# Kernel tuning notes

Hardware: AMD Instinct MI355X
Metric: run time of the kernel (lower is better)

## Reference

```python
import jax, jax.numpy as jnp
import numpy as np

DIM, HEADS = 1024, 16
B, N = 2, 2048


def setup_inputs() -> dict:
    key = jax.random.key(0)
    ks = jax.random.split(key, 8)
    d = DIM // HEADS
    return {
        "x": jax.random.normal(ks[0], (B, N, DIM), dtype=jnp.float32),
        "w_qkv": jax.random.normal(ks[1], (DIM, 3 * DIM), dtype=jnp.float32) * (DIM ** -0.5),
        "w_out": jax.random.normal(ks[2], (DIM, DIM), dtype=jnp.float32) * (DIM ** -0.5),
        "b_out": jnp.zeros((DIM,), dtype=jnp.float32),
        "void_q": jax.random.normal(ks[3], (1, HEADS, 1, d), dtype=jnp.float32),
        "void_k": jax.random.normal(ks[4], (1, HEADS, 1, d), dtype=jnp.float32),
        "void_v": jax.random.normal(ks[5], (1, HEADS, 1, d), dtype=jnp.float32),
        "attention_trace": jax.random.uniform(ks[6], (HEADS, 1, 1), dtype=jnp.float32),
        "temperature_factor": jax.random.normal(ks[7], (HEADS, 1, 1), dtype=jnp.float32),
    }


def reference(x, w_qkv, w_out, b_out, void_q, void_k, void_v,
              attention_trace, temperature_factor):
    b, n, dim = x.shape
    h = void_q.shape[1]
    d = dim // h

    qkv = x @ w_qkv  # [b, n, 3*dim]
    q, k, v = jnp.split(qkv, 3, axis=-1)

    def to_heads(t):
        return t.reshape(b, n, h, d).transpose(0, 2, 1, 3)  # b h n d

    q, k, v = to_heads(q), to_heads(k), to_heads(v)

    # append the void token to q, k, v -> seq length n+1
    q = jnp.concatenate([q, jnp.broadcast_to(void_q, (b, h, 1, d))], axis=2)
    k = jnp.concatenate([k, jnp.broadcast_to(void_k, (b, h, 1, d))], axis=2)
    v = jnp.concatenate([v, jnp.broadcast_to(void_v, (b, h, 1, d))], axis=2)

    # NOTE: original scales by full dim**-0.5, not head-dim
    dots = jnp.einsum('bhid,bhjd->bhij', q, k) * (dim ** -0.5)
    # void-to-void bias of +10 at index [n, n]
    dots = dots.at[:, :, n, n].add(10.0)

    # stateful per-head temperature (trace is a buffer, treated as input)
    temperature = jnp.maximum(1.0 + jnp.abs(attention_trace) * temperature_factor, 1.0)  # [h,1,1]
    attn = jax.nn.softmax(dots / temperature, axis=-1)  # [b, h, n+1, n+1]

    out = jnp.einsum('bhij,bhjd->bhid', attn, v)[:, :, :n, :]  # drop void row
    out = out.transpose(0, 2, 1, 3).reshape(b, n, dim)  # b n (h d)
    return out @ w_out + b_out
```

## Files before the change

### kernel.cpp

```cpp
#include <hip/hip_runtime.h>
#include <stdint.h>

#define DIMF   1024
#define HEADS  16
#define HD     64
#define BB     2
#define NN     2048
#define NKP    2112
#define NTILE  33

typedef __attribute__((ext_vector_type(8))) __bf16 bf16x8;
typedef __attribute__((ext_vector_type(4))) float  f32x4;

__device__ __forceinline__ float b2f(uint16_t h) {
  union { uint32_t u; float f; } v; v.u = ((uint32_t)h) << 16; return v.f;
}
__device__ __forceinline__ uint16_t f2b(float f) {
  union { float f; uint32_t u; } v; v.f = f;
  uint32_t r = v.u + 0x7FFFu + ((v.u >> 16) & 1u);
  return (uint16_t)(r >> 16);
}

__device__ __forceinline__ void gl_lds16(const void* g, void* l) {
  __builtin_amdgcn_global_load_lds(
      (const __attribute__((address_space(1))) void*)g,
      (__attribute__((address_space(3))) void*)l, 16, 0, 0);
}

__global__ __launch_bounds__(256) void cvt_f32_bf16(const float* __restrict__ src,
                                                    uint16_t* __restrict__ dst, int n4) {
  int i = blockIdx.x * 256 + threadIdx.x;
  if (i < n4) {
    float4 v = *(const float4*)&src[i * 4];
    uint16_t* d = dst + i * 4;
    d[0] = f2b(v.x); d[1] = f2b(v.y); d[2] = f2b(v.z); d[3] = f2b(v.w);
  }
}

__global__ __launch_bounds__(256) void transpose_k(const float* __restrict__ src,
                                                   uint16_t* __restrict__ dst, int M, int N) {
  __shared__ uint16_t tile[32][33];
  int bx = blockIdx.x * 32, by = blockIdx.y * 32;
  int x = threadIdx.x, y0 = threadIdx.y;
#pragma unroll
  for (int i = 0; i < 32; i += 8)
    tile[y0 + i][x] = f2b(src[(size_t)(by + y0 + i) * N + bx + x]);
  __syncthreads();
#pragma unroll
  for (int i = 0; i < 32; i += 8)
    dst[(size_t)(bx + y0 + i) * M + by + x] = tile[x][y0 + i];
}

__global__ __launch_bounds__(256) void fill_void(const float* __restrict__ vk,
                                                 const float* __restrict__ vv,
                                                 uint16_t* __restrict__ k_ws,
                                                 uint16_t* __restrict__ vt_ws) {
  int idx = blockIdx.x * 256 + threadIdx.x;
  int dd = idx & 63;
  int r  = (idx >> 6) & 63;
  int bh = idx >> 12;
  int h  = bh & (HEADS - 1);
  uint16_t kv  = (r == 0) ? f2b(vk[h * HD + dd]) : (uint16_t)0;
  uint16_t vvv = (r == 0) ? f2b(vv[h * HD + dd]) : (uint16_t)0;
  k_ws[((size_t)bh * NKP + NN + r) * HD + dd]  = kv;
  vt_ws[((size_t)bh * HD + dd) * NKP + NN + r] = vvv;
}

template<int EPI>
__global__ __launch_bounds__(256) void gemm_bt(const uint16_t* __restrict__ A,
                                               const uint16_t* __restrict__ Bt,
                                               int K, int Nout,
                                               uint16_t* __restrict__ o0,
                                               uint16_t* __restrict__ o1,
                                               uint16_t* __restrict__ o2,
                                               float* __restrict__ fo,
                                               const float* __restrict__ bias) {
  __shared__ uint16_t lds_a[128][32];
  __shared__ uint16_t lds_b[128][32];
  const int m0 = blockIdx.y * 128, n0 = blockIdx.x * 128;
  const int tid = threadIdx.x, lane = tid & 63, wid = tid >> 6;
  const int wm = (wid >> 1) * 64, wn = (wid & 1) * 64;
  const int lr = lane & 15, lg = lane >> 4;
  f32x4 acc[4][4] = {};
  for (int k0 = 0; k0 < K; k0 += 32) {
    __syncthreads();
#pragma unroll
    for (int it = 0; it < 2; ++it) {
      const int chunk = wid * 2 + it;
      const int o = chunk * 1024 + lane * 16;
      const int r = o >> 6, cb = o & 63;
      gl_lds16((const char*)&A[(size_t)(m0 + r) * K + k0] + cb,
               (char*)&lds_a[0][0] + chunk * 1024);
      gl_lds16((const char*)&Bt[(size_t)(n0 + r) * K + k0] + cb,
               (char*)&lds_b[0][0] + chunk * 1024);
    }
    __syncthreads();
    bf16x8 af[4], bf[4];
#pragma unroll
    for (int i = 0; i < 4; ++i)
      af[i] = *(const bf16x8*)((const char*)&lds_a[0][0] + (wm + i * 16 + lr) * 64 + lg * 16);
#pragma unroll
    for (int j = 0; j < 4; ++j)
      bf[j] = *(const bf16x8*)((const char*)&lds_b[0][0] + (wn + j * 16 + lr) * 64 + lg * 16);
#pragma unroll
    for (int i = 0; i < 4; ++i)
#pragma unroll
      for (int j = 0; j < 4; ++j)
        acc[i][j] = __builtin_amdgcn_mfma_f32_16x16x32_bf16(af[i], bf[j], acc[i][j], 0, 0, 0);
  }
#pragma unroll
  for (int i = 0; i < 4; ++i)
#pragma unroll
    for (int j = 0; j < 4; ++j)
#pragma unroll
      for (int r = 0; r < 4; ++r) {
        int mg = m0 + wm + i * 16 + lg * 4 + r;
        int ng = n0 + wn + j * 16 + lr;
        float v = acc[i][j][r];
        if (EPI == 0) {
          int b = mg >> 11, n = mg & (NN - 1);
          int which = ng >> 10, rem = ng & (DIMF - 1), h = rem >> 6, dd = rem & 63;
          int bh = b * HEADS + h;
          uint16_t bv = f2b(v);
          if (which == 0)      o0[((size_t)bh * NN + n) * HD + dd] = bv;
          else if (which == 1) o1[((size_t)bh * NKP + n) * HD + dd] = bv;
          else                 o2[((size_t)bh * HD + dd) * NKP + n] = bv;
        } else {
          fo[(size_t)mg * Nout + ng] = v + bias[ng];
        }
      }
}

__global__ __launch_bounds__(256) void attn_k(const uint16_t* __restrict__ q_ws,
                                              const uint16_t* __restrict__ k_ws,
                                              const uint16_t* __restrict__ vt_ws,
                                              const float* __restrict__ trace,
                                              const float* __restrict__ factor,
                                              uint16_t* __restrict__ o_ws) {
  __shared__ uint16_t ldsk[64][64];
  __shared__ uint16_t ldsv[64][64];
  __shared__ uint16_t ldsp[4][16][72];
  const int qb = blockIdx.x, h = blockIdx.y, b = blockIdx.z;
  const int bh = b * HEADS + h;
  const int tid = threadIdx.x, lane = tid & 63, wid = tid >> 6;
  const int lr = lane & 15, lg = lane >> 4;

  const float temp  = fmaxf(1.0f + fabsf(trace[h]) * factor[h], 1.0f);
  const float scale = 0.03125f / temp;

  const int qrow0 = qb * 64 + wid * 16;
  const uint16_t* qrow = q_ws + ((size_t)bh * NN + qrow0 + lr) * HD;
  bf16x8 qf[2];
  qf[0] = *(const bf16x8*)(qrow + lg * 8);
  qf[1] = *(const bf16x8*)(qrow + 32 + lg * 8);

  f32x4 acc[4] = {};
  float lsum[4] = {0.f, 0.f, 0.f, 0.f};

  for (int t = 0; t < NTILE; ++t) {
    const int t0 = t * 64;
    __syncthreads();
#pragma unroll
    for (int it = 0; it < 2; ++it) {
      const int chunk = wid * 2 + it;
      const int o = chunk * 1024 + lane * 16;
      const int r = o >> 7, cb = o & 127;
      const int scb = cb ^ ((r & 7) << 4);
      gl_lds16((const char*)&k_ws[((size_t)bh * NKP + t0 + r) * HD] + scb,
               (char*)&ldsk[0][0] + chunk * 1024);
      gl_lds16((const char*)&vt_ws[((size_t)bh * HD + r) * NKP + t0] + scb,
               (char*)&ldsv[0][0] + chunk * 1024);
    }
    __syncthreads();

    f32x4 s[4];
#pragma unroll
    for (int c = 0; c < 4; ++c) {
      f32x4 sa = {};
#pragma unroll
      for (int kk = 0; kk < 2; ++kk) {
        const int row = c * 16 + lr;
        const int cbb = (kk * 64 + lg * 16) ^ ((row & 7) << 4);
        bf16x8 kf = *(const bf16x8*)((const char*)&ldsk[0][0] + row * 128 + cbb);
        sa = __builtin_amdgcn_mfma_f32_16x16x32_bf16(qf[kk], kf, sa, 0, 0, 0);
      }
      s[c] = sa;
    }
#pragma unroll
    for (int c = 0; c < 4; ++c)
#pragma unroll
      for (int r = 0; r < 4; ++r) {
        float p = __expf(s[c][r] * scale);
        lsum[r] += p;
        ldsp[wid][lg * 4 + r][c * 16 + lr] = f2b(p);
      }
    asm volatile("" ::: "memory");
    __builtin_amdgcn_sched_barrier(0);
#pragma unroll
    for (int kk = 0; kk < 2; ++kk) {
      bf16x8 pf = *(const bf16x8*)&ldsp[wid][lr][kk * 32 + lg * 8];
#pragma unroll
      for (int cd = 0; cd < 4; ++cd) {
        const int row = cd * 16 + lr;
        const int cbb = (kk * 64 + lg * 16) ^ ((row & 7) << 4);
        bf16x8 vf = *(const bf16x8*)((const char*)&ldsv[0][0] + row * 128 + cbb);
        acc[cd] = __builtin_amdgcn_mfma_f32_16x16x32_bf16(pf, vf, acc[cd], 0, 0, 0);
      }
    }
  }
#pragma unroll
  for (int r = 0; r < 4; ++r) {
    float l = lsum[r];
    l += __shfl_xor(l, 1); l += __shfl_xor(l, 2);
    l += __shfl_xor(l, 4); l += __shfl_xor(l, 8);
    l -= 63.0f;
    const float inv = 1.0f / l;
    const int n = qrow0 + lg * 4 + r;
    size_t base = ((size_t)b * NN + n) * DIMF + h * HD;
#pragma unroll
    for (int cd = 0; cd < 4; ++cd)
      o_ws[base + cd * 16 + lr] = f2b(acc[cd][r] * inv);
  }
}

extern "C" void kernel_launch(void* const* d_in, const int* in_sizes, int n_in,
                              void* d_out, int out_size, void* d_ws, size_t ws_size,
                              hipStream_t stream) {
  const float* x      = (const float*)d_in[0];
  const float* wqkv   = (const float*)d_in[1];
  const float* wout   = (const float*)d_in[2];
  const float* bout   = (const float*)d_in[3];
  const float* voidk  = (const float*)d_in[5];
  const float* voidv  = (const float*)d_in[6];
  const float* trace  = (const float*)d_in[7];
  const float* factor = (const float*)d_in[8];
  float* out = (float*)d_out;

  uint16_t* ws    = (uint16_t*)d_ws;
  uint16_t* x_bf  = ws;
  uint16_t* o_ws  = x_bf;
  uint16_t* wqkvT = x_bf  + 4194304;
  uint16_t* woutT = wqkvT + 3145728;
  uint16_t* q_ws  = woutT + 1048576;
  uint16_t* k_ws  = q_ws  + 4194304;
  uint16_t* vt_ws = k_ws  + 4325376;

  cvt_f32_bf16<<<dim3(4194304 / 4 / 256), dim3(256), 0, stream>>>(x, x_bf, 4194304 / 4);
  transpose_k<<<dim3(3072 / 32, 1024 / 32), dim3(32, 8), 0, stream>>>(wqkv, wqkvT, 1024, 3072);
  transpose_k<<<dim3(1024 / 32, 1024 / 32), dim3(32, 8), 0, stream>>>(wout, woutT, 1024, 1024);
  fill_void<<<dim3(512), dim3(256), 0, stream>>>(voidk, voidv, k_ws, vt_ws);
  gemm_bt<0><<<dim3(3072 / 128, 4096 / 128), dim3(256), 0, stream>>>(
      x_bf, wqkvT, 1024, 3072, q_ws, k_ws, vt_ws, nullptr, nullptr);
  attn_k<<<dim3(NN / 64, HEADS, BB), dim3(256), 0, stream>>>(
      q_ws, k_ws, vt_ws, trace, factor, o_ws);
  gemm_bt<1><<<dim3(1024 / 128, 4096 / 128), dim3(256), 0, stream>>>(
      o_ws, woutT, 1024, 1024, nullptr, nullptr, nullptr, out, bout);
}
```

Before: 161.1 us.

## Double-buffer K/V tiles and process 32 query rows per wave in attention

The attention kernel now double-buffers K and V^T tiles in LDS, prefetching the next tile while the current one is computed, so each iteration needs one barrier instead of two. Each wave handles two 16-row query groups, which halves the grid and reuses each K/V fragment loaded from LDS across twice as many MFMAs. The QK^T product is transposed (K as the A operand) so each lane owns whole P rows, allowing packed bf16x2 stores and a single row-sum reduction. exp is replaced by exp2 with a pre-folded log2e. The cost is more LDS and registers per block and fewer blocks, which may lower occupancy.

```diff
diff --git a/kernel.cpp b/kernel.cpp
--- a/kernel.cpp
+++ b/kernel.cpp
@@ -1,4 +1,5 @@
 #include <hip/hip_runtime.h>
+#include <hip/hip_bf16.h>
 #include <stdint.h>
 
 #define DIMF   1024
@@ -19,6 +20,10 @@
   union { float f; uint32_t u; } v; v.f = f;
   uint32_t r = v.u + 0x7FFFu + ((v.u >> 16) & 1u);
   return (uint16_t)(r >> 16);
+}
+__device__ __forceinline__ uint32_t pack2(float a, float b) {
+  __hip_bfloat162 h = __float22bfloat162_rn(float2{a, b});
+  union { __hip_bfloat162 h; uint32_t u; } v; v.h = h; return v.u;
 }
 
 __device__ __forceinline__ void gl_lds16(const void* g, void* l) {
@@ -137,89 +142,115 @@
                                               const float* __restrict__ trace,
                                               const float* __restrict__ factor,
                                               uint16_t* __restrict__ o_ws) {
-  __shared__ uint16_t ldsk[64][64];
-  __shared__ uint16_t ldsv[64][64];
-  __shared__ uint16_t ldsp[4][16][72];
+  __shared__ uint16_t ldsk[2][64][64];
+  __shared__ uint16_t ldsv[2][64][64];
+  __shared__ uint16_t ldsp[4][2][16][72];
   const int qb = blockIdx.x, h = blockIdx.y, b = blockIdx.z;
   const int bh = b * HEADS + h;
   const int tid = threadIdx.x, lane = tid & 63, wid = tid >> 6;
   const int lr = lane & 15, lg = lane >> 4;
 
-  const float temp  = fmaxf(1.0f + fabsf(trace[h]) * factor[h], 1.0f);
-  const float scale = 0.03125f / temp;
-
-  const int qrow0 = qb * 64 + wid * 16;
-  const uint16_t* qrow = q_ws + ((size_t)bh * NN + qrow0 + lr) * HD;
-  bf16x8 qf[2];
-  qf[0] = *(const bf16x8*)(qrow + lg * 8);
-  qf[1] = *(const bf16x8*)(qrow + 32 + lg * 8);
-
-  f32x4 acc[4] = {};
-  float lsum[4] = {0.f, 0.f, 0.f, 0.f};
-
+  const float temp = fmaxf(1.0f + fabsf(trace[h]) * factor[h], 1.0f);
+  const float sl2  = (0.03125f / temp) * 1.44269504f;
+
+  const int qrow0 = qb * 128 + wid * 32;
+  const uint16_t* qpa = q_ws + ((size_t)bh * NN + qrow0 + lr) * HD;
+  const uint16_t* qpb = qpa + 16 * HD;
+  bf16x8 qfa[2], qfb[2];
+#pragma unroll
+  for (int kk = 0; kk < 2; ++kk) {
+    qfa[kk] = *(const bf16x8*)(qpa + kk * 32 + lg * 8);
+    qfb[kk] = *(const bf16x8*)(qpb + kk * 32 + lg * 8);
+  }
+
+  f32x4 acca[4] = {}, accb[4] = {};
+  float lsa = 0.f, lsb = 0.f;
+
+#define STAGE(buf, t)                                                              \
+  {                                                                                \
+    const int t0_ = (t) * 64;                                                      \
+    _Pragma("unroll")                                                              \
+    for (int it = 0; it < 2; ++it) {                                               \
+      const int chunk = wid * 2 + it;                                              \
+      const int o = chunk * 1024 + lane * 16;                                      \
+      const int r = o >> 7, cb = o & 127;                                          \
+      const int scb = cb ^ ((r & 7) << 4);                                         \
+      gl_lds16((const char*)&k_ws[((size_t)bh * NKP + t0_ + r) * HD] + scb,        \
+               (char*)&ldsk[buf][0][0] + chunk * 1024);                            \
+      gl_lds16((const char*)&vt_ws[((size_t)bh * HD + r) * NKP + t0_] + scb,       \
+               (char*)&ldsv[buf][0][0] + chunk * 1024);                            \
+    }                                                                              \
+  }
+
+  STAGE(0, 0);
+  __syncthreads();
+
+  int cur = 0;
   for (int t = 0; t < NTILE; ++t) {
-    const int t0 = t * 64;
-    __syncthreads();
-#pragma unroll
-    for (int it = 0; it < 2; ++it) {
-      const int chunk = wid * 2 + it;
-      const int o = chunk * 1024 + lane * 16;
-      const int r = o >> 7, cb = o & 127;
-      const int scb = cb ^ ((r & 7) << 4);
-      gl_lds16((const char*)&k_ws[((size_t)bh * NKP + t0 + r) * HD] + scb,
-               (char*)&ldsk[0][0] + chunk * 1024);
-      gl_lds16((const char*)&vt_ws[((size_t)bh * HD + r) * NKP + t0] + scb,
-               (char*)&ldsv[0][0] + chunk * 1024);
-    }
-    __syncthreads();
-
-    f32x4 s[4];
+    const int tn = (t + 1 < NTILE) ? t + 1 : t;
+    STAGE(cur ^ 1, tn);
+
 #pragma unroll
     for (int c = 0; c < 4; ++c) {
-      f32x4 sa = {};
-#pragma unroll
-      for (int kk = 0; kk < 2; ++kk) {
+      bf16x8 kf0, kf1;
+      {
         const int row = c * 16 + lr;
-        const int cbb = (kk * 64 + lg * 16) ^ ((row & 7) << 4);
-        bf16x8 kf = *(const bf16x8*)((const char*)&ldsk[0][0] + row * 128 + cbb);
-        sa = __builtin_amdgcn_mfma_f32_16x16x32_bf16(qf[kk], kf, sa, 0, 0, 0);
+        const int rsw = (row & 7) << 4;
+        kf0 = *(const bf16x8*)((const char*)&ldsk[cur][0][0] + row * 128 + ((lg * 16) ^ rsw));
+        kf1 = *(const bf16x8*)((const char*)&ldsk[cur][0][0] + row * 128 + ((64 + lg * 16) ^ rsw));
       }
-      s[c] = sa;
-    }
-#pragma unroll
-    for (int c = 0; c < 4; ++c)
-#pragma unroll
-      for (int r = 0; r < 4; ++r) {
-        float p = __expf(s[c][r] * scale);
-        lsum[r] += p;
-        ldsp[wid][lg * 4 + r][c * 16 + lr] = f2b(p);
-      }
+      f32x4 sa = {}, sb = {};
+      sa = __builtin_amdgcn_mfma_f32_16x16x32_bf16(kf0, qfa[0], sa, 0, 0, 0);
+      sa = __builtin_amdgcn_mfma_f32_16x16x32_bf16(kf1, qfa[1], sa, 0, 0, 0);
+      sb = __builtin_amdgcn_mfma_f32_16x16x32_bf16(kf0, qfb[0], sb, 0, 0, 0);
+      sb = __builtin_amdgcn_mfma_f32_16x16x32_bf16(kf1, qfb[1], sb, 0, 0, 0);
+      float p0 = exp2f(sa[0] * sl2), p1 = exp2f(sa[1] * sl2);
+      float p2 = exp2f(sa[2] * sl2), p3 = exp2f(sa[3] * sl2);
+      lsa += (p0 + p1) + (p2 + p3);
+      *(uint32_t*)&ldsp[wid][0][lr][c * 16 + lg * 4]     = pack2(p0, p1);
+      *(uint32_t*)&ldsp[wid][0][lr][c * 16 + lg * 4 + 2] = pack2(p2, p3);
+      p0 = exp2f(sb[0] * sl2); p1 = exp2f(sb[1] * sl2);
+      p2 = exp2f(sb[2] * sl2); p3 = exp2f(sb[3] * sl2);
+      lsb += (p0 + p1) + (p2 + p3);
+      *(uint32_t*)&ldsp[wid][1][lr][c * 16 + lg * 4]     = pack2(p0, p1);
+      *(uint32_t*)&ldsp[wid][1][lr][c * 16 + lg * 4 + 2] = pack2(p2, p3);
+    }
     asm volatile("" ::: "memory");
     __builtin_amdgcn_sched_barrier(0);
+
 #pragma unroll
     for (int kk = 0; kk < 2; ++kk) {
-      bf16x8 pf = *(const bf16x8*)&ldsp[wid][lr][kk * 32 + lg * 8];
+      bf16x8 pfa = *(const bf16x8*)&ldsp[wid][0][lr][kk * 32 + lg * 8];
+      bf16x8 pfb = *(const bf16x8*)&ldsp[wid][1][lr][kk * 32 + lg * 8];
 #pragma unroll
       for (int cd = 0; cd < 4; ++cd) {
         const int row = cd * 16 + lr;
         const int cbb = (kk * 64 + lg * 16) ^ ((row & 7) << 4);
-        bf16x8 vf = *(const bf16x8*)((const char*)&ldsv[0][0] + row * 128 + cbb);
-        acc[cd] = __builtin_amdgcn_mfma_f32_16x16x32_bf16(pf, vf, acc[cd], 0, 0, 0);
+        bf16x8 vf = *(const bf16x8*)((const char*)&ldsv[cur][0][0] + row * 128 + cbb);
+        acca[cd] = __builtin_amdgcn_mfma_f32_16x16x32_bf16(pfa, vf, acca[cd], 0, 0, 0);
+        accb[cd] = __builtin_amdgcn_mfma_f32_16x16x32_bf16(pfb, vf, accb[cd], 0, 0, 0);
       }
     }
-  }
+    __syncthreads();
+    cur ^= 1;
+  }
+
+  lsa += __shfl_xor(lsa, 16); lsa += __shfl_xor(lsa, 32);
+  lsb += __shfl_xor(lsb, 16); lsb += __shfl_xor(lsb, 32);
+
 #pragma unroll
   for (int r = 0; r < 4; ++r) {
-    float l = lsum[r];
-    l += __shfl_xor(l, 1); l += __shfl_xor(l, 2);
-    l += __shfl_xor(l, 4); l += __shfl_xor(l, 8);
-    l -= 63.0f;
-    const float inv = 1.0f / l;
-    const int n = qrow0 + lg * 4 + r;
-    size_t base = ((size_t)b * NN + n) * DIMF + h * HD;
-#pragma unroll
-    for (int cd = 0; cd < 4; ++cd)
-      o_ws[base + cd * 16 + lr] = f2b(acc[cd][r] * inv);
+    const int src = lg * 4 + r;
+    const float inva = 1.0f / (__shfl(lsa, src) - 63.0f);
+    const float invb = 1.0f / (__shfl(lsb, src) - 63.0f);
+    const int na = qrow0 + lg * 4 + r;
+    size_t basea = ((size_t)b * NN + na) * DIMF + h * HD;
+    size_t baseb = basea + (size_t)16 * DIMF;
+#pragma unroll
+    for (int cd = 0; cd < 4; ++cd) {
+      o_ws[basea + cd * 16 + lr] = f2b(acca[cd][r] * inva);
+      o_ws[baseb + cd * 16 + lr] = f2b(accb[cd][r] * invb);
+    }
   }
 }
 
@@ -251,7 +282,7 @@
   fill_void<<<dim3(512), dim3(256), 0, stream>>>(voidk, voidv, k_ws, vt_ws);
   gemm_bt<0><<<dim3(3072 / 128, 4096 / 128), dim3(256), 0, stream>>>(
       x_bf, wqkvT, 1024, 3072, q_ws, k_ws, vt_ws, nullptr, nullptr);
-  attn_k<<<dim3(NN / 64, HEADS, BB), dim3(256), 0, stream>>>(
+  attn_k<<<dim3(NN / 128, HEADS, BB), dim3(256), 0, stream>>>(
       q_ws, k_ws, vt_ws, trace, factor, o_ws);
   gemm_bt<1><<<dim3(1024 / 128, 4096 / 128), dim3(256), 0, stream>>>(
       o_ws, woutT, 1024, 1024, nullptr, nullptr, nullptr, out, bout);
```

After: 170.6 us. 5.9% more time.

## Fold softmax scale into Q projection epilogue and transpose score MFMA

Applied to the files above, without the earlier changes.

The QKV GEMM epilogue now multiplies Q by the softmax scale (including log2(e) and the per-head temperature), so the attention kernel can call exp2f directly with no per-element multiply. The score MFMA swaps its operands so each lane holds four consecutive keys of one query row. That lets probabilities be stored as packed bf16 pairs and the row sum be reduced with two shuffles instead of four per row. Rounding the scaled Q to bf16 slightly changes numerics, and the GEMM epilogue gains a small per-element branch with two extra loads.

```diff
diff --git a/kernel.cpp b/kernel.cpp
--- a/kernel.cpp
+++ b/kernel.cpp
@@ -1,4 +1,5 @@
 #include <hip/hip_runtime.h>
+#include <hip/hip_bf16.h>
 #include <stdint.h>
 
 #define DIMF   1024
@@ -19,6 +20,10 @@
   union { float f; uint32_t u; } v; v.f = f;
   uint32_t r = v.u + 0x7FFFu + ((v.u >> 16) & 1u);
   return (uint16_t)(r >> 16);
+}
+__device__ __forceinline__ uint32_t pack2(float a, float b) {
+  __hip_bfloat162 h = __float22bfloat162_rn(float2{a, b});
+  union { __hip_bfloat162 h; uint32_t u; } v; v.h = h; return v.u;
 }
 
 __device__ __forceinline__ void gl_lds16(const void* g, void* l) {
@@ -74,7 +79,9 @@
                                                uint16_t* __restrict__ o1,
                                                uint16_t* __restrict__ o2,
                                                float* __restrict__ fo,
-                                               const float* __restrict__ bias) {
+                                               const float* __restrict__ bias,
+                                               const float* __restrict__ trace,
+                                               const float* __restrict__ factor) {
   __shared__ uint16_t lds_a[128][32];
   __shared__ uint16_t lds_b[128][32];
   const int m0 = blockIdx.y * 128, n0 = blockIdx.x * 128;
@@ -121,7 +128,12 @@
           int b = mg >> 11, n = mg & (NN - 1);
           int which = ng >> 10, rem = ng & (DIMF - 1), h = rem >> 6, dd = rem & 63;
           int bh = b * HEADS + h;
-          uint16_t bv = f2b(v);
+          float vv = v;
+          if (which == 0) {
+            float tmp = fmaxf(1.0f + fabsf(trace[h]) * factor[h], 1.0f);
+            vv = v * (0.04508422f / tmp);
+          }
+          uint16_t bv = f2b(vv);
           if (which == 0)      o0[((size_t)bh * NN + n) * HD + dd] = bv;
           else if (which == 1) o1[((size_t)bh * NKP + n) * HD + dd] = bv;
           else                 o2[((size_t)bh * HD + dd) * NKP + n] = bv;
@@ -134,8 +146,6 @@
 __global__ __launch_bounds__(256) void attn_k(const uint16_t* __restrict__ q_ws,
                                               const uint16_t* __restrict__ k_ws,
                                               const uint16_t* __restrict__ vt_ws,
-                                              const float* __restrict__ trace,
-                                              const float* __restrict__ factor,
                                               uint16_t* __restrict__ o_ws) {
   __shared__ uint16_t ldsk[64][64];
   __shared__ uint16_t ldsv[64][64];
@@ -145,17 +155,14 @@
   const int tid = threadIdx.x, lane = tid & 63, wid = tid >> 6;
   const int lr = lane & 15, lg = lane >> 4;
 
-  const float temp  = fmaxf(1.0f + fabsf(trace[h]) * factor[h], 1.0f);
-  const float scale = 0.03125f / temp;
-
   const int qrow0 = qb * 64 + wid * 16;
-  const uint16_t* qrow = q_ws + ((size_t)bh * NN + qrow0 + lr) * HD;
+  const uint16_t* qp = q_ws + ((size_t)bh * NN + qrow0 + lr) * HD;
   bf16x8 qf[2];
-  qf[0] = *(const bf16x8*)(qrow + lg * 8);
-  qf[1] = *(const bf16x8*)(qrow + 32 + lg * 8);
+  qf[0] = *(const bf16x8*)(qp + lg * 8);
+  qf[1] = *(const bf16x8*)(qp + 32 + lg * 8);
 
   f32x4 acc[4] = {};
-  float lsum[4] = {0.f, 0.f, 0.f, 0.f};
+  float lsum = 0.f;
 
   for (int t = 0; t < NTILE; ++t) {
     const int t0 = t * 64;
@@ -173,29 +180,24 @@
     }
     __syncthreads();
 
-    f32x4 s[4];
 #pragma unroll
     for (int c = 0; c < 4; ++c) {
-      f32x4 sa = {};
-#pragma unroll
-      for (int kk = 0; kk < 2; ++kk) {
-        const int row = c * 16 + lr;
-        const int cbb = (kk * 64 + lg * 16) ^ ((row & 7) << 4);
-        bf16x8 kf = *(const bf16x8*)((const char*)&ldsk[0][0] + row * 128 + cbb);
-        sa = __builtin_amdgcn_mfma_f32_16x16x32_bf16(qf[kk], kf, sa, 0, 0, 0);
-      }
-      s[c] = sa;
-    }
-#pragma unroll
-    for (int c = 0; c < 4; ++c)
-#pragma unroll
-      for (int r = 0; r < 4; ++r) {
-        float p = __expf(s[c][r] * scale);
-        lsum[r] += p;
-        ldsp[wid][lg * 4 + r][c * 16 + lr] = f2b(p);
-      }
+      const int row = c * 16 + lr;
+      const int rsw = (row & 7) << 4;
+      bf16x8 kf0 = *(const bf16x8*)((const char*)&ldsk[0][0] + row * 128 + ((lg * 16) ^ rsw));
+      bf16x8 kf1 = *(const bf16x8*)((const char*)&ldsk[0][0] + row * 128 + ((64 + lg * 16) ^ rsw));
+      f32x4 s = {};
+      s = __builtin_amdgcn_mfma_f32_16x16x32_bf16(kf0, qf[0], s, 0, 0, 0);
+      s = __builtin_amdgcn_mfma_f32_16x16x32_bf16(kf1, qf[1], s, 0, 0, 0);
+      float p0 = exp2f(s[0]), p1 = exp2f(s[1]);
+      float p2 = exp2f(s[2]), p3 = exp2f(s[3]);
+      lsum += (p0 + p1) + (p2 + p3);
+      *(uint32_t*)&ldsp[wid][lr][c * 16 + lg * 4]     = pack2(p0, p1);
+      *(uint32_t*)&ldsp[wid][lr][c * 16 + lg * 4 + 2] = pack2(p2, p3);
+    }
     asm volatile("" ::: "memory");
     __builtin_amdgcn_sched_barrier(0);
+
 #pragma unroll
     for (int kk = 0; kk < 2; ++kk) {
       bf16x8 pf = *(const bf16x8*)&ldsp[wid][lr][kk * 32 + lg * 8];
@@ -208,15 +210,15 @@
       }
     }
   }
+
+  lsum += __shfl_xor(lsum, 16); lsum += __shfl_xor(lsum, 32);
+
 #pragma unroll
   for (int r = 0; r < 4; ++r) {
-    float l = lsum[r];
-    l += __shfl_xor(l, 1); l += __shfl_xor(l, 2);
-    l += __shfl_xor(l, 4); l += __shfl_xor(l, 8);
-    l -= 63.0f;
-    const float inv = 1.0f / l;
-    const int n = qrow0 + lg * 4 + r;
-    size_t base = ((size_t)b * NN + n) * DIMF + h * HD;
+    const int src = lg * 4 + r;
+    const float inv = 1.0f / (__shfl(lsum, src) - 63.0f);
+    const int na = qrow0 + lg * 4 + r;
+    size_t base = ((size_t)b * NN + na) * DIMF + h * HD;
 #pragma unroll
     for (int cd = 0; cd < 4; ++cd)
       o_ws[base + cd * 16 + lr] = f2b(acc[cd][r] * inv);
@@ -250,9 +252,8 @@
   transpose_k<<<dim3(1024 / 32, 1024 / 32), dim3(32, 8), 0, stream>>>(wout, woutT, 1024, 1024);
   fill_void<<<dim3(512), dim3(256), 0, stream>>>(voidk, voidv, k_ws, vt_ws);
   gemm_bt<0><<<dim3(3072 / 128, 4096 / 128), dim3(256), 0, stream>>>(
-      x_bf, wqkvT, 1024, 3072, q_ws, k_ws, vt_ws, nullptr, nullptr);
-  attn_k<<<dim3(NN / 64, HEADS, BB), dim3(256), 0, stream>>>(
-      q_ws, k_ws, vt_ws, trace, factor, o_ws);
+      x_bf, wqkvT, 1024, 3072, q_ws, k_ws, vt_ws, nullptr, nullptr, trace, factor);
+  attn_k<<<dim3(NN / 64, HEADS, BB), dim3(256), 0, stream>>>(q_ws, k_ws, vt_ws, o_ws);
   gemm_bt<1><<<dim3(1024 / 128, 4096 / 128), dim3(256), 0, stream>>>(
-      o_ws, woutT, 1024, 1024, nullptr, nullptr, nullptr, out, bout);
-}
+      o_ws, woutT, 1024, 1024, nullptr, nullptr, nullptr, out, bout, nullptr, nullptr);
+}
```

Measured after the change: 177.3 us. 1.1x slower.
